# Optimization experiments

Hardware: AMD Instinct MI355X
Metric: run time of the kernel (lower is better)

The kernel has to match this reference:

```python
import jax, jax.numpy as jnp
import numpy as np

N_NODES = 100000
N_EDGES = 1600000
N_GRAPHS = 256
NEG_SLOPE_GAT = 0.2   # GATConv default
NEG_SLOPE_ACT = 0.01  # F.leaky_relu default


def _leaky(x, s):
    return jnp.where(x >= 0, x, s * x)


def _gat_layer(x, src, dst, W, a_src, a_dst, b, n):
    # h = W x ; per-node attention logits
    h = x @ W                      # [N, D]
    al_s = h @ a_src               # [N]
    al_d = h @ a_dst               # [N]
    e = _leaky(al_s[src] + al_d[dst], NEG_SLOPE_GAT)  # [E]
    # segment softmax over incoming edges of each dst node
    m = jax.ops.segment_max(e, dst, num_segments=n)
    m = jnp.where(jnp.isfinite(m), m, 0.0)
    ex = jnp.exp(e - m[dst])
    s = jax.ops.segment_sum(ex, dst, num_segments=n)
    alpha = ex / (s[dst] + 1e-16)
    out = jax.ops.segment_sum(h[src] * alpha[:, None], dst, num_segments=n)
    return out + b


def setup_inputs() -> dict:
    key = jax.random.key(0)
    ks = jax.random.split(key, 12)
    x = jax.random.normal(ks[0], (N_NODES, 72), dtype=jnp.float32)
    edge_index = jax.random.randint(ks[1], (2, N_EDGES), 0, N_NODES, dtype=jnp.int64)
    batch = jnp.sort(jax.random.randint(ks[2], (N_NODES,), 0, N_GRAPHS, dtype=jnp.int64))
    def glorot(k, shape):
        fan = shape[0] + shape[-1]
        return jax.random.normal(k, shape, dtype=jnp.float32) * jnp.sqrt(2.0 / fan)
    return {
        "x": x, "edge_index": edge_index, "batch": batch,
        "W1": glorot(ks[3], (72, 64)),
        "a_src1": glorot(ks[4], (64,)), "a_dst1": glorot(ks[5], (64,)),
        "b1": jnp.zeros((64,), jnp.float32),
        "W2": glorot(ks[6], (64, 64)),
        "a_src2": glorot(ks[7], (64,)), "a_dst2": glorot(ks[8], (64,)),
        "b2": jnp.zeros((64,), jnp.float32),
        "fcW": glorot(ks[9], (64, 2)),
        "fcb": jnp.zeros((2,), jnp.float32),
    }


def reference(x, edge_index, batch, W1, a_src1, a_dst1, b1, W2, a_src2, a_dst2, b2, fcW, fcb):
    n = x.shape[0]
    # PyG GATConv adds self-loops by default
    loops = jnp.arange(n, dtype=edge_index.dtype)
    src = jnp.concatenate([edge_index[0], loops])
    dst = jnp.concatenate([edge_index[1], loops])
    h = _gat_layer(x, src, dst, W1, a_src1, a_dst1, b1, n)
    h = _leaky(h, NEG_SLOPE_ACT)
    h = _gat_layer(h, src, dst, W2, a_src2, a_dst2, b2, n)
    # global mean pool over graphs
    sums = jax.ops.segment_sum(h, batch, num_segments=N_GRAPHS)
    cnt = jax.ops.segment_sum(jnp.ones((n,), h.dtype), batch, num_segments=N_GRAPHS)
    pooled = sums / jnp.maximum(cnt, 1.0)[:, None]
    # dropout is identity at inference
    return pooled @ fcW + fcb
```

## Files before the change

kernel.cpp:

```cpp
#include <hip/hip_runtime.h>
#include <hip/hip_bf16.h>
#include <math.h>


#define NPB 256
#define EPB 4096
#define PSTRIDE 4608
#define XPAD 68

__device__ __forceinline__ unsigned int f2bf(float v) {
    unsigned int b = __float_as_uint(v);
    b += 0x7FFFu + ((b >> 16) & 1u);
    return b >> 16;
}

__global__ __launch_bounds__(256) void init_all(int* __restrict__ bcur, int NB) {
    int i = blockIdx.x * 256 + threadIdx.x;
    if (i < NB) bcur[i] = 0;
}

__global__ __launch_bounds__(256) void partition(const int* __restrict__ ei,
                                                 int E, int NB,
                                                 int* __restrict__ bcur,
                                                 unsigned int* __restrict__ pairs) {
    __shared__ int h[512];
    __shared__ int hb[512];
    int t = threadIdx.x;
    for (int i = t; i < 512; i += 256) h[i] = 0;
    __syncthreads();
    int i0 = blockIdx.x * EPB;
    unsigned int val[16];
    int bk[16], r[16];
#pragma unroll
    for (int k = 0; k < 16; k++) {
        int i = i0 + k * 256 + t;
        bk[k] = -1;
        if (i < E) {
            int s = ei[i];
            int d = ei[E + i];
            bk[k] = d >> 8;
            val[k] = (unsigned)s | ((unsigned)(d & 255) << 24);
            r[k] = atomicAdd(&h[bk[k]], 1);
        }
    }
    __syncthreads();
    for (int b = t; b < NB; b += 256)
        hb[b] = h[b] ? atomicAdd(&bcur[b], h[b]) : 0;
    __syncthreads();
#pragma unroll
    for (int k = 0; k < 16; k++) {
        if (bk[k] < 0) continue;
        int pos = hb[bk[k]] + r[k];
        if (pos < PSTRIDE)
            pairs[(size_t)bk[k] * PSTRIDE + pos] = val[k];
    }
}

__global__ __launch_bounds__(256) void build_csr(const unsigned int* __restrict__ pairs,
                                                 const int* __restrict__ bcur,
                                                 int n, int NB,
                                                 int* __restrict__ rowptr,
                                                 int* __restrict__ srcs) {
    int b = blockIdx.x, t = threadIdx.x;
    __shared__ int c[512];
    __shared__ int s2[256];
    __shared__ int sbase, stot;
    __shared__ unsigned int Q[PSTRIDE];
    __shared__ int hist[256];
    __shared__ int hcur[256];
    int c0 = (2 * t < NB) ? min(bcur[2 * t], PSTRIDE) : 0;
    int c1 = (2 * t + 1 < NB) ? min(bcur[2 * t + 1], PSTRIDE) : 0;
    c[2 * t] = c0; c[2 * t + 1] = c1;
    s2[t] = c0 + c1;
    hist[t] = 0;
    __syncthreads();
    for (int o = 1; o < 256; o <<= 1) {
        int u = (t >= o) ? s2[t - o] : 0;
        __syncthreads();
        s2[t] += u;
        __syncthreads();
    }
    if (t == 0) {
        int p = b >> 1;
        int ex = s2[p] - (c[2 * p] + c[2 * p + 1]);
        sbase = ex + ((b & 1) ? c[b & ~1] : 0);
        stot = s2[255];
    }
    __syncthreads();
    int d0 = b << 8;
    int nb = min(NPB, n - d0);
    int cnt_b = c[b];
    int csr0 = sbase + d0;
    const unsigned int* pb = pairs + (size_t)b * PSTRIDE;

    for (int j = t; j < cnt_b; j += 256)
        atomicAdd(&hist[(pb[j] & 0xFFFFFFu) >> 9], 1);
    __syncthreads();
    int hv = hist[t];
    hcur[t] = hv;
    __syncthreads();
    for (int o = 1; o < 256; o <<= 1) {
        int u = (t >= o) ? hcur[t - o] : 0;
        __syncthreads();
        hcur[t] += u;
        __syncthreads();
    }
    hcur[t] -= hv;
    __syncthreads();
    for (int j = t; j < cnt_b; j += 256) {
        unsigned int p = pb[j];
        int pos = atomicAdd(&hcur[(p & 0xFFFFFFu) >> 9], 1);
        Q[pos] = p;
    }
    __syncthreads();

    __shared__ int deg[NPB];
    __shared__ int cur[NPB];
    __shared__ int tmp[NPB];
    deg[t] = (t < nb) ? 1 : 0;
    __syncthreads();
    for (int j = t; j < cnt_b; j += 256)
        atomicAdd(&deg[Q[j] >> 24], 1);
    __syncthreads();
    int v = deg[t];
    tmp[t] = v;
    __syncthreads();
    for (int o = 1; o < NPB; o <<= 1) {
        int u = (t >= o) ? tmp[t - o] : 0;
        __syncthreads();
        tmp[t] += u;
        __syncthreads();
    }
    int excl = tmp[t] - v;
    if (t < nb) {
        rowptr[d0 + t] = csr0 + excl;
        srcs[csr0 + excl] = d0 + t;
        cur[t] = excl + 1;
    }
    __syncthreads();
    for (int j = t; j < cnt_b; j += 256) {
        unsigned int p = Q[j];
        int off = atomicAdd(&cur[p >> 24], 1);
        srcs[csr0 + off] = (int)(p & 0x00FFFFFFu);
    }
    if (b == 0 && t == 0) rowptr[n] = n + stot;
}

template <int IN_DIM>
__global__ __launch_bounds__(256) void node_gemm(const float* __restrict__ x,
                                                 const float* __restrict__ W,
                                                 const float* __restrict__ a_src,
                                                 const float* __restrict__ a_dst,
                                                 const float* __restrict__ bias_in,
                                                 float slope_in,
                                                 unsigned short* __restrict__ h16,
                                                 float* __restrict__ al_s,
                                                 float* __restrict__ al_d,
                                                 int n) {
    __shared__ float Ws[IN_DIM * 64];
    __shared__ float xs[IN_DIM][XPAD];
    int t = threadIdx.x;
    int nbase = blockIdx.x * 64;

    for (int idx = t; idx < IN_DIM * 16; idx += 256)
        ((float4*)Ws)[idx] = ((const float4*)W)[idx];
    const float* xb = x + (size_t)nbase * IN_DIM;
    int lim = min(64, n - nbase) * IN_DIM;
    for (int idx = t; idx < 64 * IN_DIM; idx += 256) {
        int node = idx / IN_DIM;
        int k = idx - node * IN_DIM;
        float v = 0.0f;
        if (idx < lim) {
            v = xb[idx];
            if (bias_in) {
                v += bias_in[k];
                v = (v >= 0.0f) ? v : slope_in * v;
            }
        }
        xs[k][node] = v;
    }
    __syncthreads();

    int cg = t & 15;
    int ng = t >> 4;
    float acc[4][4] = {};
#pragma unroll 8
    for (int k = 0; k < IN_DIM; k++) {
        float4 xv = *(const float4*)&xs[k][ng * 4];
        float4 wv = *(const float4*)&Ws[k * 64 + cg * 4];
        float xa[4] = {xv.x, xv.y, xv.z, xv.w};
        float wa[4] = {wv.x, wv.y, wv.z, wv.w};
#pragma unroll
        for (int i = 0; i < 4; i++)
#pragma unroll
            for (int j = 0; j < 4; j++)
                acc[i][j] += xa[i] * wa[j];
    }

    float4 as4 = *(const float4*)(a_src + cg * 4);
    float4 ad4 = *(const float4*)(a_dst + cg * 4);
#pragma unroll
    for (int i = 0; i < 4; i++) {
        int node = nbase + ng * 4 + i;
        if (node < n) {
            uint2 p;
            p.x = f2bf(acc[i][0]) | (f2bf(acc[i][1]) << 16);
            p.y = f2bf(acc[i][2]) | (f2bf(acc[i][3]) << 16);
            *(uint2*)(h16 + (size_t)node * 64 + cg * 4) = p;
        }
        float vs = acc[i][0] * as4.x + acc[i][1] * as4.y +
                   acc[i][2] * as4.z + acc[i][3] * as4.w;
        float vd = acc[i][0] * ad4.x + acc[i][1] * ad4.y +
                   acc[i][2] * ad4.z + acc[i][3] * ad4.w;
#pragma unroll
        for (int o = 8; o; o >>= 1) {
            vs += __shfl_xor(vs, o);
            vd += __shfl_xor(vd, o);
        }
        if (cg == 0 && node < n) { al_s[node] = vs; al_d[node] = vd; }
    }
}

__device__ __forceinline__ void bf8_fma(float* acc, uint4 q, float w) {
    acc[0] += w * __uint_as_float(q.x << 16);
    acc[1] += w * __uint_as_float(q.x & 0xFFFF0000u);
    acc[2] += w * __uint_as_float(q.y << 16);
    acc[3] += w * __uint_as_float(q.y & 0xFFFF0000u);
    acc[4] += w * __uint_as_float(q.z << 16);
    acc[5] += w * __uint_as_float(q.z & 0xFFFF0000u);
    acc[6] += w * __uint_as_float(q.w << 16);
    acc[7] += w * __uint_as_float(q.w & 0xFFFF0000u);
}

__global__ __launch_bounds__(256) void gat_aggregate(const int* __restrict__ rowptr,
                                                     const int* __restrict__ srcs,
                                                     const float* __restrict__ als,
                                                     const float* __restrict__ ald,
                                                     const unsigned short* __restrict__ h16,
                                                     float* __restrict__ hout,
                                                     int n) {
    int t = threadIdx.x;
    int sub = t >> 3, lane = t & 7;
    int node = blockIdx.x * 32 + sub;
    if (node >= n) return;
    int beg = rowptr[node], end = rowptr[node + 1];
    float aldv = ald[node];
    const unsigned short* hb = h16 + lane * 8;

    float acc[8] = {};
    float sm = 0.0f;
    int j = beg;
    if (j + 4 <= end) {
        int s0 = srcs[j], s1 = srcs[j + 1], s2 = srcs[j + 2], s3 = srcs[j + 3];
        for (; j + 8 <= end; j += 4) {
            int n0 = srcs[j + 4], n1 = srcs[j + 5];
            int n2 = srcs[j + 6], n3 = srcs[j + 7];
            float e0 = als[s0] + aldv, e1 = als[s1] + aldv;
            float e2 = als[s2] + aldv, e3 = als[s3] + aldv;
            uint4 q0 = *(const uint4*)(hb + (size_t)s0 * 64);
            uint4 q1 = *(const uint4*)(hb + (size_t)s1 * 64);
            uint4 q2 = *(const uint4*)(hb + (size_t)s2 * 64);
            uint4 q3 = *(const uint4*)(hb + (size_t)s3 * 64);
            e0 = (e0 >= 0.0f) ? e0 : 0.2f * e0;
            e1 = (e1 >= 0.0f) ? e1 : 0.2f * e1;
            e2 = (e2 >= 0.0f) ? e2 : 0.2f * e2;
            e3 = (e3 >= 0.0f) ? e3 : 0.2f * e3;
            float w0 = __expf(e0), w1 = __expf(e1);
            float w2 = __expf(e2), w3 = __expf(e3);
            sm += (w0 + w1) + (w2 + w3);
            bf8_fma(acc, q0, w0);
            bf8_fma(acc, q1, w1);
            bf8_fma(acc, q2, w2);
            bf8_fma(acc, q3, w3);
            s0 = n0; s1 = n1; s2 = n2; s3 = n3;
        }
        {
            float e0 = als[s0] + aldv, e1 = als[s1] + aldv;
            float e2 = als[s2] + aldv, e3 = als[s3] + aldv;
            uint4 q0 = *(const uint4*)(hb + (size_t)s0 * 64);
            uint4 q1 = *(const uint4*)(hb + (size_t)s1 * 64);
            uint4 q2 = *(const uint4*)(hb + (size_t)s2 * 64);
            uint4 q3 = *(const uint4*)(hb + (size_t)s3 * 64);
            e0 = (e0 >= 0.0f) ? e0 : 0.2f * e0;
            e1 = (e1 >= 0.0f) ? e1 : 0.2f * e1;
            e2 = (e2 >= 0.0f) ? e2 : 0.2f * e2;
            e3 = (e3 >= 0.0f) ? e3 : 0.2f * e3;
            float w0 = __expf(e0), w1 = __expf(e1);
            float w2 = __expf(e2), w3 = __expf(e3);
            sm += (w0 + w1) + (w2 + w3);
            bf8_fma(acc, q0, w0);
            bf8_fma(acc, q1, w1);
            bf8_fma(acc, q2, w2);
            bf8_fma(acc, q3, w3);
            j += 4;
        }
    }
    for (; j < end; j++) {
        int s = srcs[j];
        float e = als[s] + aldv;
        e = (e >= 0.0f) ? e : 0.2f * e;
        float w = __expf(e);
        uint4 q = *(const uint4*)(hb + (size_t)s * 64);
        sm += w;
        bf8_fma(acc, q, w);
    }

    float inv = 1.0f / (sm + 1e-16f);
    float4 o0 = make_float4(acc[0] * inv, acc[1] * inv, acc[2] * inv, acc[3] * inv);
    float4 o1 = make_float4(acc[4] * inv, acc[5] * inv, acc[6] * inv, acc[7] * inv);
    float* op = hout + (size_t)node * 64 + lane * 8;
    *(float4*)op = o0;
    *(float4*)(op + 4) = o1;
}

__global__ __launch_bounds__(256) void pool_fc(const float* __restrict__ hout,
                                               const float* __restrict__ b2,
                                               const int* __restrict__ batch,
                                               const float* __restrict__ fcW,
                                               const float* __restrict__ fcb,
                                               float* __restrict__ out, int n) {
    int g = blockIdx.x;
    int t = threadIdx.x;
    __shared__ int sLo, sHi;
    __shared__ float red[4][64];
    if (t == 0) {
        int lo = 0, hi = n;
        while (lo < hi) { int m = (lo + hi) >> 1; if (batch[m] < g) lo = m + 1; else hi = m; }
        sLo = lo;
    } else if (t == 64) {
        int lo = 0, hi = n;
        while (lo < hi) { int m = (lo + hi) >> 1; if (batch[m] < g + 1) lo = m + 1; else hi = m; }
        sHi = lo;
    }
    __syncthreads();
    int lo = sLo, hi = sHi;
    int wv = t >> 6, lane = t & 63;
    float acc = 0.0f;
    for (int node = lo + wv; node < hi; node += 4)
        acc += hout[(size_t)node * 64 + lane];
    red[wv][lane] = acc;
    __syncthreads();
    if (wv == 0) {
        float c = (float)(hi - lo);
        float s = red[0][lane] + red[1][lane] + red[2][lane] + red[3][lane];
        s += c * b2[lane];
        float cd = (c > 1.0f) ? c : 1.0f;
        float p = s / cd;
        float s0 = p * fcW[lane * 2 + 0];
        float s1 = p * fcW[lane * 2 + 1];
#pragma unroll
        for (int o = 32; o; o >>= 1) {
            s0 += __shfl_xor(s0, o);
            s1 += __shfl_xor(s1, o);
        }
        if (lane == 0) {
            out[g * 2 + 0] = s0 + fcb[0];
            out[g * 2 + 1] = s1 + fcb[1];
        }
    }
}

extern "C" void kernel_launch(void* const* d_in, const int* in_sizes, int n_in,
                              void* d_out, int out_size, void* d_ws, size_t ws_size,
                              hipStream_t stream) {
    const float* x    = (const float*)d_in[0];
    const int*   ei   = (const int*)d_in[1];
    const int*   batch= (const int*)d_in[2];
    const float* W1   = (const float*)d_in[3];
    const float* as1  = (const float*)d_in[4];
    const float* ad1  = (const float*)d_in[5];
    const float* b1   = (const float*)d_in[6];
    const float* W2   = (const float*)d_in[7];
    const float* as2  = (const float*)d_in[8];
    const float* ad2  = (const float*)d_in[9];
    const float* b2   = (const float*)d_in[10];
    const float* fcW  = (const float*)d_in[11];
    const float* fcb  = (const float*)d_in[12];
    float* out = (float*)d_out;

    const int N = in_sizes[2];
    const int E = in_sizes[1] / 2;
    const int G = out_size / 2;
    const int tot = E + N;
    const int NB = (N + NPB - 1) / NPB;

    float* ws     = (float*)d_ws;
    float* bufO   = ws;
    unsigned int* pairs  = (unsigned int*)bufO;
    float* als    = bufO + (size_t)N * 64;
    float* ald    = als + N;
    int*   rowptr = (int*)(ald + N);
    int*   srcs   = rowptr + N + 1;
    int*   bcur   = srcs + tot;
    unsigned short* bufH16 = (unsigned short*)(bcur + NB);

    dim3 b256(256);
    int gInit = (NB + 255) / 256;
    int gPart = (E + EPB - 1) / EPB;
    int gGemm = (N + 63) / 64;
    int gAgg  = (N + 31) / 32;

    init_all<<<gInit, b256, 0, stream>>>(bcur, NB);
    partition<<<gPart, b256, 0, stream>>>(ei, E, NB, bcur, pairs);
    build_csr<<<NB, b256, 0, stream>>>(pairs, bcur, N, NB, rowptr, srcs);

    node_gemm<72><<<gGemm, b256, 0, stream>>>(x, W1, as1, ad1, nullptr, 0.0f,
                                              bufH16, als, ald, N);
    gat_aggregate<<<gAgg, b256, 0, stream>>>(rowptr, srcs, als, ald, bufH16, bufO, N);

    node_gemm<64><<<gGemm, b256, 0, stream>>>(bufO, W2, as2, ad2, b1, 0.01f,
                                              bufH16, als, ald, N);
    gat_aggregate<<<gAgg, b256, 0, stream>>>(rowptr, srcs, als, ald, bufH16, bufO, N);

    pool_fc<<<G, b256, 0, stream>>>(bufO, b2, batch, fcW, fcb, out, N);
}
```

Baseline: 331.0 us.

## Fuse mean-pool into second GAT aggregate and deepen edge-gather unroll to 8

The second aggregation now accumulates its per-node outputs straight into per-graph sums through a block reduction plus atomics, so the 100k×64 float output is never written and pool_fc no longer re-reads it. A small 64-thread kernel then finishes the mean and the FC layer. The edge loop is restructured to issue 8 independent gathers per iteration instead of 4 with software prefetch, and the launch bounds now request 8 blocks per CU. In exchange, float atomics make the pooled sums order-nondeterministic, and the wider unroll raises register pressure.

```diff
diff --git a/kernel.cpp b/kernel.cpp
--- a/kernel.cpp
+++ b/kernel.cpp
@@ -14,9 +14,11 @@
     return b >> 16;
 }
 
-__global__ __launch_bounds__(256) void init_all(int* __restrict__ bcur, int NB) {
+__global__ __launch_bounds__(256) void init_all(int* __restrict__ bcur, int NB,
+                                                float* __restrict__ gsum, int M) {
     int i = blockIdx.x * 256 + threadIdx.x;
     if (i < NB) bcur[i] = 0;
+    if (i < M) gsum[i] = 0.0f;
 }
 
 __global__ __launch_bounds__(256) void partition(const int* __restrict__ ei,
@@ -232,68 +234,84 @@
     acc[7] += w * __uint_as_float(q.w & 0xFFFF0000u);
 }
 
-__global__ __launch_bounds__(256) void gat_aggregate(const int* __restrict__ rowptr,
-                                                     const int* __restrict__ srcs,
-                                                     const float* __restrict__ als,
-                                                     const float* __restrict__ ald,
-                                                     const unsigned short* __restrict__ h16,
-                                                     float* __restrict__ hout,
-                                                     int n) {
+template <bool POOL>
+__global__ __launch_bounds__(256, 8) void gat_aggregate(const int* __restrict__ rowptr,
+                                                        const int* __restrict__ srcs,
+                                                        const float* __restrict__ als,
+                                                        const float* __restrict__ ald,
+                                                        const unsigned short* __restrict__ h16,
+                                                        float* __restrict__ hout,
+                                                        float* __restrict__ gsum,
+                                                        const int* __restrict__ batch,
+                                                        int n) {
     int t = threadIdx.x;
     int sub = t >> 3, lane = t & 7;
     int node = blockIdx.x * 32 + sub;
-    if (node >= n) return;
-    int beg = rowptr[node], end = rowptr[node + 1];
-    float aldv = ald[node];
+    bool act = node < n;
+    int beg = 0, end = 0;
+    float aldv = 0.0f;
+    if (act) { beg = rowptr[node]; end = rowptr[node + 1]; aldv = ald[node]; }
     const unsigned short* hb = h16 + lane * 8;
 
     float acc[8] = {};
     float sm = 0.0f;
     int j = beg;
-    if (j + 4 <= end) {
+    for (; j + 8 <= end; j += 8) {
+        int s0 = srcs[j],     s1 = srcs[j + 1], s2 = srcs[j + 2], s3 = srcs[j + 3];
+        int s4 = srcs[j + 4], s5 = srcs[j + 5], s6 = srcs[j + 6], s7 = srcs[j + 7];
+        uint4 q0 = *(const uint4*)(hb + (size_t)s0 * 64);
+        uint4 q1 = *(const uint4*)(hb + (size_t)s1 * 64);
+        uint4 q2 = *(const uint4*)(hb + (size_t)s2 * 64);
+        uint4 q3 = *(const uint4*)(hb + (size_t)s3 * 64);
+        uint4 q4 = *(const uint4*)(hb + (size_t)s4 * 64);
+        uint4 q5 = *(const uint4*)(hb + (size_t)s5 * 64);
+        uint4 q6 = *(const uint4*)(hb + (size_t)s6 * 64);
+        uint4 q7 = *(const uint4*)(hb + (size_t)s7 * 64);
+        float e0 = als[s0] + aldv, e1 = als[s1] + aldv;
+        float e2 = als[s2] + aldv, e3 = als[s3] + aldv;
+        float e4 = als[s4] + aldv, e5 = als[s5] + aldv;
+        float e6 = als[s6] + aldv, e7 = als[s7] + aldv;
+        e0 = (e0 >= 0.0f) ? e0 : 0.2f * e0;
+        e1 = (e1 >= 0.0f) ? e1 : 0.2f * e1;
+        e2 = (e2 >= 0.0f) ? e2 : 0.2f * e2;
+        e3 = (e3 >= 0.0f) ? e3 : 0.2f * e3;
+        e4 = (e4 >= 0.0f) ? e4 : 0.2f * e4;
+        e5 = (e5 >= 0.0f) ? e5 : 0.2f * e5;
+        e6 = (e6 >= 0.0f) ? e6 : 0.2f * e6;
+        e7 = (e7 >= 0.0f) ? e7 : 0.2f * e7;
+        float w0 = __expf(e0), w1 = __expf(e1);
+        float w2 = __expf(e2), w3 = __expf(e3);
+        float w4 = __expf(e4), w5 = __expf(e5);
+        float w6 = __expf(e6), w7 = __expf(e7);
+        sm += ((w0 + w1) + (w2 + w3)) + ((w4 + w5) + (w6 + w7));
+        bf8_fma(acc, q0, w0);
+        bf8_fma(acc, q1, w1);
+        bf8_fma(acc, q2, w2);
+        bf8_fma(acc, q3, w3);
+        bf8_fma(acc, q4, w4);
+        bf8_fma(acc, q5, w5);
+        bf8_fma(acc, q6, w6);
+        bf8_fma(acc, q7, w7);
+    }
+    for (; j + 4 <= end; j += 4) {
         int s0 = srcs[j], s1 = srcs[j + 1], s2 = srcs[j + 2], s3 = srcs[j + 3];
-        for (; j + 8 <= end; j += 4) {
-            int n0 = srcs[j + 4], n1 = srcs[j + 5];
-            int n2 = srcs[j + 6], n3 = srcs[j + 7];
-            float e0 = als[s0] + aldv, e1 = als[s1] + aldv;
-            float e2 = als[s2] + aldv, e3 = als[s3] + aldv;
-            uint4 q0 = *(const uint4*)(hb + (size_t)s0 * 64);
-            uint4 q1 = *(const uint4*)(hb + (size_t)s1 * 64);
-            uint4 q2 = *(const uint4*)(hb + (size_t)s2 * 64);
-            uint4 q3 = *(const uint4*)(hb + (size_t)s3 * 64);
-            e0 = (e0 >= 0.0f) ? e0 : 0.2f * e0;
-            e1 = (e1 >= 0.0f) ? e1 : 0.2f * e1;
-            e2 = (e2 >= 0.0f) ? e2 : 0.2f * e2;
-            e3 = (e3 >= 0.0f) ? e3 : 0.2f * e3;
-            float w0 = __expf(e0), w1 = __expf(e1);
-            float w2 = __expf(e2), w3 = __expf(e3);
-            sm += (w0 + w1) + (w2 + w3);
-            bf8_fma(acc, q0, w0);
-            bf8_fma(acc, q1, w1);
-            bf8_fma(acc, q2, w2);
-            bf8_fma(acc, q3, w3);
-            s0 = n0; s1 = n1; s2 = n2; s3 = n3;
-        }
-        {
-            float e0 = als[s0] + aldv, e1 = als[s1] + aldv;
-            float e2 = als[s2] + aldv, e3 = als[s3] + aldv;
-            uint4 q0 = *(const uint4*)(hb + (size_t)s0 * 64);
-            uint4 q1 = *(const uint4*)(hb + (size_t)s1 * 64);
-            uint4 q2 = *(const uint4*)(hb + (size_t)s2 * 64);
-            uint4 q3 = *(const uint4*)(hb + (size_t)s3 * 64);
-            e0 = (e0 >= 0.0f) ? e0 : 0.2f * e0;
-            e1 = (e1 >= 0.0f) ? e1 : 0.2f * e1;
-            e2 = (e2 >= 0.0f) ? e2 : 0.2f * e2;
-            e3 = (e3 >= 0.0f) ? e3 : 0.2f * e3;
-            float w0 = __expf(e0), w1 = __expf(e1);
-            float w2 = __expf(e2), w3 = __expf(e3);
-            sm += (w0 + w1) + (w2 + w3);
-            bf8_fma(acc, q0, w0);
-            bf8_fma(acc, q1, w1);
-            bf8_fma(acc, q2, w2);
-            bf8_fma(acc, q3, w3);
-            j += 4;
-        }
+        uint4 q0 = *(const uint4*)(hb + (size_t)s0 * 64);
+        uint4 q1 = *(const uint4*)(hb + (size_t)s1 * 64);
+        uint4 q2 = *(const uint4*)(hb + (size_t)s2 * 64);
+        uint4 q3 = *(const uint4*)(hb + (size_t)s3 * 64);
+        float e0 = als[s0] + aldv, e1 = als[s1] + aldv;
+        float e2 = als[s2] + aldv, e3 = als[s3] + aldv;
+        e0 = (e0 >= 0.0f) ? e0 : 0.2f * e0;
+        e1 = (e1 >= 0.0f) ? e1 : 0.2f * e1;
+        e2 = (e2 >= 0.0f) ? e2 : 0.2f * e2;
+        e3 = (e3 >= 0.0f) ? e3 : 0.2f * e3;
+        float w0 = __expf(e0), w1 = __expf(e1);
+        float w2 = __expf(e2), w3 = __expf(e3);
+        sm += (w0 + w1) + (w2 + w3);
+        bf8_fma(acc, q0, w0);
+        bf8_fma(acc, q1, w1);
+        bf8_fma(acc, q2, w2);
+        bf8_fma(acc, q3, w3);
     }
     for (; j < end; j++) {
         int s = srcs[j];
@@ -306,14 +324,47 @@
     }
 
     float inv = 1.0f / (sm + 1e-16f);
-    float4 o0 = make_float4(acc[0] * inv, acc[1] * inv, acc[2] * inv, acc[3] * inv);
-    float4 o1 = make_float4(acc[4] * inv, acc[5] * inv, acc[6] * inv, acc[7] * inv);
-    float* op = hout + (size_t)node * 64 + lane * 8;
-    *(float4*)op = o0;
-    *(float4*)(op + 4) = o1;
-}
-
-__global__ __launch_bounds__(256) void pool_fc(const float* __restrict__ hout,
+    if (!POOL) {
+        if (act) {
+            float* op = hout + (size_t)node * 64 + lane * 8;
+            *(float4*)op = make_float4(acc[0] * inv, acc[1] * inv, acc[2] * inv, acc[3] * inv);
+            *(float4*)(op + 4) = make_float4(acc[4] * inv, acc[5] * inv, acc[6] * inv, acc[7] * inv);
+        }
+    } else {
+        float o[8];
+#pragma unroll
+        for (int k = 0; k < 8; k++) o[k] = act ? acc[k] * inv : 0.0f;
+        int d0 = blockIdx.x * 32;
+        int gF = batch[d0];
+        int gL = batch[(d0 + 31 < n) ? d0 + 31 : n - 1];
+        __shared__ float red[4][64];
+        if (gF == gL) {
+#pragma unroll
+            for (int k = 0; k < 8; k++) {
+                o[k] += __shfl_xor(o[k], 8);
+                o[k] += __shfl_xor(o[k], 16);
+                o[k] += __shfl_xor(o[k], 32);
+            }
+            int wv = t >> 6;
+            if ((t & 56) == 0) {
+#pragma unroll
+                for (int k = 0; k < 8; k++) red[wv][lane * 8 + k] = o[k];
+            }
+            __syncthreads();
+            if (t < 64) {
+                float s = red[0][t] + red[1][t] + red[2][t] + red[3][t];
+                atomicAdd(&gsum[gF * 64 + t], s);
+            }
+        } else {
+            int myg = act ? batch[node] : gF;
+#pragma unroll
+            for (int k = 0; k < 8; k++)
+                atomicAdd(&gsum[myg * 64 + lane * 8 + k], o[k]);
+        }
+    }
+}
+
+__global__ __launch_bounds__(64) void fc_small(const float* __restrict__ gsum,
                                                const float* __restrict__ b2,
                                                const int* __restrict__ batch,
                                                const float* __restrict__ fcW,
@@ -322,41 +373,30 @@
     int g = blockIdx.x;
     int t = threadIdx.x;
     __shared__ int sLo, sHi;
-    __shared__ float red[4][64];
     if (t == 0) {
         int lo = 0, hi = n;
         while (lo < hi) { int m = (lo + hi) >> 1; if (batch[m] < g) lo = m + 1; else hi = m; }
         sLo = lo;
-    } else if (t == 64) {
+    } else if (t == 1) {
         int lo = 0, hi = n;
         while (lo < hi) { int m = (lo + hi) >> 1; if (batch[m] < g + 1) lo = m + 1; else hi = m; }
         sHi = lo;
     }
     __syncthreads();
-    int lo = sLo, hi = sHi;
-    int wv = t >> 6, lane = t & 63;
-    float acc = 0.0f;
-    for (int node = lo + wv; node < hi; node += 4)
-        acc += hout[(size_t)node * 64 + lane];
-    red[wv][lane] = acc;
-    __syncthreads();
-    if (wv == 0) {
-        float c = (float)(hi - lo);
-        float s = red[0][lane] + red[1][lane] + red[2][lane] + red[3][lane];
-        s += c * b2[lane];
-        float cd = (c > 1.0f) ? c : 1.0f;
-        float p = s / cd;
-        float s0 = p * fcW[lane * 2 + 0];
-        float s1 = p * fcW[lane * 2 + 1];
-#pragma unroll
-        for (int o = 32; o; o >>= 1) {
-            s0 += __shfl_xor(s0, o);
-            s1 += __shfl_xor(s1, o);
-        }
-        if (lane == 0) {
-            out[g * 2 + 0] = s0 + fcb[0];
-            out[g * 2 + 1] = s1 + fcb[1];
-        }
+    float c = (float)(sHi - sLo);
+    float s = gsum[g * 64 + t] + c * b2[t];
+    float cd = (c > 1.0f) ? c : 1.0f;
+    float p = s / cd;
+    float s0 = p * fcW[t * 2 + 0];
+    float s1 = p * fcW[t * 2 + 1];
+#pragma unroll
+    for (int o = 32; o; o >>= 1) {
+        s0 += __shfl_xor(s0, o);
+        s1 += __shfl_xor(s1, o);
+    }
+    if (t == 0) {
+        out[g * 2 + 0] = s0 + fcb[0];
+        out[g * 2 + 1] = s1 + fcb[1];
     }
 }
 
@@ -393,24 +433,28 @@
     int*   srcs   = rowptr + N + 1;
     int*   bcur   = srcs + tot;
     unsigned short* bufH16 = (unsigned short*)(bcur + NB);
+    float* gsum   = (float*)(bufH16 + (size_t)N * 64);
 
     dim3 b256(256);
-    int gInit = (NB + 255) / 256;
+    int gsElems = G * 64;
+    int gInit = (max(NB, gsElems) + 255) / 256;
     int gPart = (E + EPB - 1) / EPB;
     int gGemm = (N + 63) / 64;
     int gAgg  = (N + 31) / 32;
 
-    init_all<<<gInit, b256, 0, stream>>>(bcur, NB);
+    init_all<<<gInit, b256, 0, stream>>>(bcur, NB, gsum, gsElems);
     partition<<<gPart, b256, 0, stream>>>(ei, E, NB, bcur, pairs);
     build_csr<<<NB, b256, 0, stream>>>(pairs, bcur, N, NB, rowptr, srcs);
 
     node_gemm<72><<<gGemm, b256, 0, stream>>>(x, W1, as1, ad1, nullptr, 0.0f,
                                               bufH16, als, ald, N);
-    gat_aggregate<<<gAgg, b256, 0, stream>>>(rowptr, srcs, als, ald, bufH16, bufO, N);
+    gat_aggregate<false><<<gAgg, b256, 0, stream>>>(rowptr, srcs, als, ald,
+                                                    bufH16, bufO, nullptr, nullptr, N);
 
     node_gemm<64><<<gGemm, b256, 0, stream>>>(bufO, W2, as2, ad2, b1, 0.01f,
                                               bufH16, als, ald, N);
-    gat_aggregate<<<gAgg, b256, 0, stream>>>(rowptr, srcs, als, ald, bufH16, bufO, N);
-
-    pool_fc<<<G, b256, 0, stream>>>(bufO, b2, batch, fcW, fcb, out, N);
-}
+    gat_aggregate<true><<<gAgg, b256, 0, stream>>>(rowptr, srcs, als, ald,
+                                                   bufH16, nullptr, gsum, batch, N);
+
+    fc_small<<<G, dim3(64), 0, stream>>>(gsum, b2, batch, fcW, fcb, out, N);
+}
```

Measured after the change: 411.6 us. 1.24x slower.
